# Kernel tuning notes

Hardware: AMD Instinct MI355X
Metric: run time of the kernel (lower is better)

The kernel has to match this reference:

```python
import jax, jax.numpy as jnp
import numpy as np

N_TAPS = 5
N_DELAY = 1
N_ITER = 2
REF_MIC = 0
EPS = 1e-3        # eps passed to ISS updates / divisions
MODEL_EPS = 1e-5  # LaplaceModel internal eps
PB_EPS = 1e-6     # projection_back eps


def _mag_sq(x):
    return jnp.real(x) ** 2 + jnp.imag(x) ** 2


def _div(num, den, eps=EPS):
    # torchiva divide: num / clamp(den, min=eps); den is real
    return num / jnp.maximum(den, eps)


def _laplace_model(Y):
    # Laplace source model: per-source/per-frame weight 1/(2*||y(:,n)||), broadcast over freq
    denom = 2.0 * jnp.sqrt(jnp.sum(_mag_sq(Y), axis=-2, keepdims=True))
    return jnp.broadcast_to(1.0 / jnp.maximum(denom, MODEL_EPS), Y.shape)


def _demix_derev(X, X_bar, W, H):
    reverb = jnp.einsum('...cfdt,...dftn->...cfn', H, X_bar)
    sep = jnp.einsum('...cfd,...dfn->...cfn', W, X)
    return sep - reverb


def _background_update(W, H, C_XX, C_XbarX):
    n_src = W.shape[-3]
    A = (jnp.einsum('...sfc,...cfd->...fsd', W, C_XX)
         + jnp.einsum('...sfdt,...dtfc->...fsc', H, C_XbarX))
    J_H = jnp.linalg.solve(A[..., :n_src], A[..., n_src:])  # (..., f, s, c-s)
    return jnp.moveaxis(jnp.conj(J_H), -1, -3)              # (..., c-s, f, s)


def _demix_background(X, J):
    n_src = J.shape[-1]
    return jnp.einsum('...cfd,...dfn->...cfn', J, X[..., :n_src, :, :]) - X[..., n_src:, :, :]


def _iss_v1(src, X, weights, eps=EPS):
    n_frames = X.shape[-1]
    Xs = X[..., src, :, :]
    v_num = jnp.einsum('...cfn,...cfn,...fn->...cf', weights, X, jnp.conj(Xs)) / n_frames
    v_den = jnp.einsum('...cfn,...fn->...cf', weights, _mag_sq(Xs)) / n_frames
    v = _div(v_num, v_den, eps)
    v_s = 1.0 - 1.0 / jnp.sqrt(jnp.maximum(v_den[..., src, :], eps))
    return v.at[..., src, :].set(v_s.astype(v.dtype))


def _iss_v23(X, Zs, weights, eps=EPS):
    v_num = jnp.einsum('...cfn,...cfn,...fn->...cf', weights, X, jnp.conj(Zs))
    v_den = jnp.einsum('...cfn,...fn->...cf', weights, _mag_sq(Zs))
    return _div(v_num, v_den, eps)


def _iss_updates_with_H(X, X_bar, W, H, weights, J=None, Z=None, eps=EPS):
    n_src = X.shape[-3]
    n_chan = n_src if J is None else n_src + Z.shape[-3]
    n_taps = X_bar.shape[-2]
    # sequential rank-1 source updates (loop-carried; small fixed trip count)
    for src in range(n_src):
        v = _iss_v1(src, X, weights, eps)
        X = X - jnp.einsum('...cf,...fn->...cfn', v, X[..., src, :, :])
        W = W - jnp.einsum('...cf,...fd->...cfd', v, W[..., src, :, :])
        H = H - jnp.einsum('...cf,...fdt->...cfdt', v, H[..., src, :, :, :])
    if Z is not None and J is not None:
        for bak in range(n_chan - n_src):
            v = _iss_v23(X, Z[..., bak, :, :], weights, eps)
            X = X - jnp.einsum('...cf,...fn->...cfn', v, Z[..., bak, :, :])
            W = W.at[..., :n_src].add(-jnp.einsum('...cf,...fd->...cfd', v, J[..., bak, :, :]))
            W = W.at[..., n_src + bak].add(v)
    for src in range(n_chan):
        for tap in range(n_taps):
            Xst = X_bar[..., src, :, tap, :]
            v = _iss_v23(X, Xst, weights, eps)
            X = X - jnp.einsum('...cf,...fn->...cfn', v, Xst)
            H = H.at[..., src, tap].add(v)
    return X, W, H


def _one_iter(Y, X, X_bar, C_XX, C_XbarX, W, H, J, eps=EPS):
    weights = _laplace_model(Y)
    g = jnp.maximum(jnp.mean(_mag_sq(Y), axis=(-2, -1), keepdims=True), eps)
    g_sqrt = jnp.sqrt(g)
    Y = _div(Y, g_sqrt, eps)
    W = _div(W, g_sqrt, eps)
    H = _div(H, g_sqrt[..., None], eps)
    weights = weights * g
    J = _background_update(W, H, C_XX, C_XbarX)
    Z = _demix_background(X, J)
    Y, W, H = _iss_updates_with_H(Y, X_bar, W, H, weights, J=J, Z=Z, eps=eps)
    return Y, W, H, J


def _projection_back(Y, W, J, ref_mic=REF_MIC, eps=PB_EPS):
    # overdetermined branch (n_src < n_chan), ref_mic < n_src
    n_src = Y.shape[-3]
    eye = jnp.eye(n_src, dtype=W.dtype)
    W1, W2 = W[..., :n_src], W[..., n_src:]
    B = jnp.einsum('...sfc,...cfk->...sfk', W2, J) + W1  # (..., s, f, s)
    rhs = eye[:, ref_mic:ref_mic + 1]                    # (s, 1)
    BT = jnp.einsum('...sfc->...fcs', B)                 # (..., f, s, s)
    rhs_b = jnp.broadcast_to(rhs, BT.shape[:-2] + rhs.shape)
    a = jnp.linalg.solve(BT + eps * eye, rhs_b)          # (..., f, s, 1)
    a = jnp.swapaxes(a, -3, -2)                          # (..., s, f, 1)
    return Y * a


def _forward(X, n_src):
    n_chan, n_freq, n_frames = X.shape[-3:]
    batch = X.shape[:-3]
    # delayed copies: X_bar[..., c, f, t, n] = X_pad[..., c, f, n + t]
    X_pad = jnp.pad(X, [(0, 0)] * (X.ndim - 1) + [(N_TAPS + N_DELAY, 0)])
    X_bar = jnp.stack([X_pad[..., t:t + n_frames] for t in range(N_TAPS)], axis=-2)
    C_XX = jnp.einsum('...cfn,...dfn->...cfd', X, jnp.conj(X)) / n_frames
    C_XbarX = jnp.einsum('...dftn,...cfn->...dtfc', X_bar, jnp.conj(X)) / n_frames
    eye = jnp.eye(n_chan, dtype=X.dtype)[:n_src]
    W = jnp.broadcast_to(eye[:, None, :], batch + (n_src, n_freq, n_chan))
    H = jnp.zeros(batch + (n_src, n_freq, n_chan, N_TAPS), dtype=X.dtype)
    J = jnp.zeros(batch + (n_chan - n_src, n_freq, n_src), dtype=X.dtype)
    Y = X[..., :n_src, :, :]
    for _ in range(N_ITER):
        Y, W, H, J = _one_iter(Y, X, X_bar, C_XX, C_XbarX, W, H, J)
    J = _background_update(W, H, C_XX, C_XbarX)
    Y = _demix_derev(X, X_bar, W, H)
    Y = _projection_back(Y, W, J)
    return Y


def setup_inputs():
    key = jax.random.key(0)
    k1, k2 = jax.random.split(key)
    B, n_chan, n_freq, n_frames = 2, 6, 257, 1000
    X_real = jax.random.normal(k1, (B, n_chan, n_freq, n_frames), dtype=jnp.float32)
    X_imag = jax.random.normal(k2, (B, n_chan, n_freq, n_frames), dtype=jnp.float32)
    return {"X_real": X_real, "X_imag": X_imag, "n_src": 2}


def reference(X_real, X_imag, n_src):
    X = jax.lax.complex(X_real, X_imag)
    Y = _forward(X, n_src)  # (B, n_src, n_freq, n_frames) complex
    # real view of the complex output: last axis = (real, imag)
    return jnp.stack([jnp.real(Y), jnp.imag(Y)], axis=-1)
```

## Files before the change

kernel.cpp:

```cpp
#include <hip/hip_runtime.h>
#include <math.h>

#define F_   257
#define N_   1000
#define C_   6
#define S_   2
#define K_   4
#define T_   5
#define DLY  6
#define EPSF 1e-3f
#define MODEL_EPSF 1e-5f
#define PB_EPSD 1e-6
#define NTHR 512

__device__ __forceinline__ float2 cmul(float2 a, float2 b){
  return make_float2(a.x*b.x - a.y*b.y, a.x*b.y + a.y*b.x);
}
__device__ __forceinline__ float2 cadd(float2 a, float2 b){ return make_float2(a.x+b.x, a.y+b.y); }
__device__ __forceinline__ float2 csub(float2 a, float2 b){ return make_float2(a.x-b.x, a.y-b.y); }

struct dc { double x, y; };
__device__ __forceinline__ dc dmul(dc a, dc b){ return dc{a.x*b.x - a.y*b.y, a.x*b.y + a.y*b.x}; }
__device__ __forceinline__ dc dadd(dc a, dc b){ return dc{a.x+b.x, a.y+b.y}; }
__device__ __forceinline__ dc dsub(dc a, dc b){ return dc{a.x-b.x, a.y-b.y}; }
__device__ __forceinline__ dc ddiv(dc a, dc b){
  double d = b.x*b.x + b.y*b.y;
  return dc{(a.x*b.x + a.y*b.y)/d, (a.y*b.x - a.x*b.y)/d};
}
__device__ __forceinline__ dc d_of(float2 a){ return dc{(double)a.x, (double)a.y}; }

struct V2 { float2 v0, v1; };

__global__ __launch_bounds__(128) void k_weights_x(const float* __restrict__ Xre,
    const float* __restrict__ Xim, float* __restrict__ deng, float* __restrict__ gsumg)
{
  __shared__ float redw[2];
  int blk = blockIdx.x;
  int fc = blk & 15; int ch = (blk >> 4) & 7; int s = (blk >> 7) & 1; int b = blk >> 8;
  int tid = threadIdx.x;
  int n = ch*125 + tid;
  int f0 = fc*17, f1 = (f0 + 17 < F_) ? f0 + 17 : F_;
  float acc = 0.f;
  if (tid < 125){
    for (int f = f0; f < f1; ++f){
      size_t gi = ((size_t)(b*C_+s)*F_ + f)*N_ + n;
      float xr = Xre[gi], xi = Xim[gi];
      acc += xr*xr + xi*xi;
    }
    atomicAdd(&deng[(b*S_+s)*N_ + n], acc);
  }
  float r = (tid < 125) ? acc : 0.f;
  #pragma unroll
  for (int off = 32; off; off >>= 1) r += __shfl_xor(r, off);
  if ((tid & 63) == 0) redw[tid >> 6] = r;
  __syncthreads();
  if (tid == 0) atomicAdd(&gsumg[b*S_+s], redw[0] + redw[1]);
}

__global__ __launch_bounds__(128) void k_weights_y(const float2* __restrict__ Yg,
    float* __restrict__ deng, float* __restrict__ gsumg)
{
  __shared__ float redw[2];
  int blk = blockIdx.x;
  int fc = blk & 15; int ch = (blk >> 4) & 7; int s = (blk >> 7) & 1; int b = blk >> 8;
  int tid = threadIdx.x;
  int n = ch*125 + tid;
  int f0 = fc*17, f1 = (f0 + 17 < F_) ? f0 + 17 : F_;
  float acc = 0.f;
  if (tid < 125){
    for (int f = f0; f < f1; ++f){
      float2 y = Yg[(((size_t)(b*F_+f))*S_ + s)*N_ + n];
      acc += y.x*y.x + y.y*y.y;
    }
    atomicAdd(&deng[(b*S_+s)*N_ + n], acc);
  }
  float r = (tid < 125) ? acc : 0.f;
  #pragma unroll
  for (int off = 32; off; off >>= 1) r += __shfl_xor(r, off);
  if ((tid & 63) == 0) redw[tid >> 6] = r;
  __syncthreads();
  if (tid == 0) atomicAdd(&gsumg[b*S_+s], redw[0] + redw[1]);
}

__device__ __forceinline__ void bg_update(int tid, const float2* Wl,
    const float2* Hl, float2* Al, float2* Jl,
    const float2* cx, const float2* cb)
{
  if (tid < S_*C_){
    int s = tid / C_, j = tid - s*C_;
    float2 a = make_float2(0.f, 0.f);
    #pragma unroll
    for (int i = 0; i < C_; ++i) a = cadd(a, cmul(Wl[s*C_+i], cx[i*C_+j]));
    #pragma unroll
    for (int i = 0; i < C_; ++i)
      #pragma unroll
      for (int t = 0; t < T_; ++t)
        a = cadd(a, cmul(Hl[(s*C_+i)*T_+t], cb[(i*T_+t)*C_+j]));
    Al[s*C_+j] = a;
  }
  __syncthreads();
  if (tid == 0){
    dc M00 = d_of(Al[0]),  M01 = d_of(Al[1]);
    dc M10 = d_of(Al[C_]), M11 = d_of(Al[C_+1]);
    dc det = dsub(dmul(M00, M11), dmul(M01, M10));
    #pragma unroll
    for (int k = 0; k < K_; ++k){
      dc r0 = d_of(Al[2+k]), r1 = d_of(Al[C_+2+k]);
      dc x0 = ddiv(dsub(dmul(M11, r0), dmul(M01, r1)), det);
      dc x1 = ddiv(dsub(dmul(M00, r1), dmul(M10, r0)), det);
      Jl[k*S_+0] = make_float2((float)x0.x, (float)(-x0.y));
      Jl[k*S_+1] = make_float2((float)x1.x, (float)(-x1.y));
    }
  }
  __syncthreads();
}

template<typename FS>
__device__ __forceinline__ V2 round2(int tid, bool hasB, int rb, float* redl,
    float2& yA0, float2& yA1, float2& yB0, float2& yB1,
    float wA0, float wA1, float wB0, float wB1,
    FS sf, bool isV1, int src)
{
  float2 sA = sf(0), sB = sf(1);
  float m = sA.x*sA.x + sA.y*sA.y;
  float r0 = wA0*(yA0.x*sA.x + yA0.y*sA.y);
  float r1 = wA0*(yA0.y*sA.x - yA0.x*sA.y);
  float r2 = wA0*m;
  float r3 = wA1*(yA1.x*sA.x + yA1.y*sA.y);
  float r4 = wA1*(yA1.y*sA.x - yA1.x*sA.y);
  float r5 = wA1*m;
  if (hasB){
    float mb = sB.x*sB.x + sB.y*sB.y;
    r0 += wB0*(yB0.x*sB.x + yB0.y*sB.y);
    r1 += wB0*(yB0.y*sB.x - yB0.x*sB.y);
    r2 += wB0*mb;
    r3 += wB1*(yB1.x*sB.x + yB1.y*sB.y);
    r4 += wB1*(yB1.y*sB.x - yB1.x*sB.y);
    r5 += wB1*mb;
  }
  #pragma unroll
  for (int off = 32; off; off >>= 1){
    r0 += __shfl_xor(r0, off); r1 += __shfl_xor(r1, off);
    r2 += __shfl_xor(r2, off); r3 += __shfl_xor(r3, off);
    r4 += __shfl_xor(r4, off); r5 += __shfl_xor(r5, off);
  }
  int lane = tid & 63, wid = tid >> 6;
  if (lane == 0){
    float2* rw = (float2*)(redl + rb*64 + wid*8);
    rw[0] = make_float2(r0, r1);
    rw[1] = make_float2(r2, r3);
    rw[2] = make_float2(r4, r5);
  }
  __syncthreads();
  float pv = ((lane & 7) < 6) ? redl[rb*64 + (lane >> 3)*8 + (lane & 7)] : 0.f;
  pv += __shfl_xor(pv, 8);
  pv += __shfl_xor(pv, 16);
  pv += __shfl_xor(pv, 32);
  float t0 = __shfl(pv, 0), t1 = __shfl(pv, 1), t2 = __shfl(pv, 2);
  float t3 = __shfl(pv, 3), t4 = __shfl(pv, 4), t5 = __shfl(pv, 5);
  if (isV1){
    const float inv = 1.f/(float)N_;
    t0*=inv; t1*=inv; t2*=inv; t3*=inv; t4*=inv; t5*=inv;
  }
  float d0 = fmaxf(t2, EPSF), d1 = fmaxf(t5, EPSF);
  float2 v0 = make_float2(t0/d0, t1/d0);
  float2 v1 = make_float2(t3/d1, t4/d1);
  if (isV1){
    if (src == 0) v0 = make_float2(1.f - 1.f/sqrtf(d0), 0.f);
    else          v1 = make_float2(1.f - 1.f/sqrtf(d1), 0.f);
  }
  yA0 = csub(yA0, cmul(v0, sA)); yA1 = csub(yA1, cmul(v1, sA));
  if (hasB){ yB0 = csub(yB0, cmul(v0, sB)); yB1 = csub(yB1, cmul(v1, sB)); }
  return V2{v0, v1};
}

template<bool FIRST, bool FINAL>
__global__ __launch_bounds__(512, 6) void k_main(const float* __restrict__ Xre,
    const float* __restrict__ Xim, float2* __restrict__ Yg, float2* __restrict__ Wg,
    float2* __restrict__ Hg, float2* __restrict__ Cxxg,
    float2* __restrict__ Cbxg, const float* __restrict__ deng,
    const float* __restrict__ gsumg, float2* __restrict__ out2)
{
  __shared__ float2 Xl[C_*N_];
  __shared__ float2 Wl[S_*C_];
  __shared__ float2 Hl[S_*C_*T_];
  __shared__ float2 Jl[K_*S_];
  __shared__ float2 Al[S_*C_];
  __shared__ float  redl[2*64];
  __shared__ float2 Cxl[C_*C_];
  __shared__ float2 Cbl[C_*T_*C_];

  int p = blockIdx.x; int b = p / F_; int f = p - b*F_;
  int tid = threadIdx.x;
  const int nA = tid;
  const int nB = tid + NTHR;
  const bool hasB = (nB < N_);
  const int nBs = hasB ? nB : 0;

  for (int i = tid; i < C_*N_; i += NTHR){
    int c = i / N_, n = i - c*N_;
    size_t gi = ((size_t)(b*C_+c)*F_ + f)*N_ + n;
    Xl[i] = make_float2(Xre[gi], Xim[gi]);
  }
  if (tid < 128) redl[tid] = 0.f;

  float gv0 = fmaxf(gsumg[b*S_+0] * (1.f/((float)F_*(float)N_)), EPSF);
  float gv1 = fmaxf(gsumg[b*S_+1] * (1.f/((float)F_*(float)N_)), EPSF);
  float ig0 = 1.f / fmaxf(sqrtf(gv0), EPSF);
  float ig1 = 1.f / fmaxf(sqrtf(gv1), EPSF);

  float wA0 = gv0 / fmaxf(2.f*sqrtf(deng[(b*S_+0)*N_+nA]), MODEL_EPSF);
  float wA1 = gv1 / fmaxf(2.f*sqrtf(deng[(b*S_+1)*N_+nA]), MODEL_EPSF);
  float wB0 = 0.f, wB1 = 0.f;
  if (hasB){
    wB0 = gv0 / fmaxf(2.f*sqrtf(deng[(b*S_+0)*N_+nB]), MODEL_EPSF);
    wB1 = gv1 / fmaxf(2.f*sqrtf(deng[(b*S_+1)*N_+nB]), MODEL_EPSF);
  }

  if (FIRST){
    if (tid < S_*C_){
      int s = tid / C_, c = tid - s*C_;
      Wl[tid] = make_float2((s==c) ? (s ? ig1 : ig0) : 0.f, 0.f);
    }
    if (tid < S_*C_*T_) Hl[tid] = make_float2(0.f, 0.f);
  } else {
    if (tid < S_*C_){
      float ig = (tid / C_) ? ig1 : ig0;
      float2 w = Wg[(size_t)p*S_*C_ + tid];
      Wl[tid] = make_float2(w.x*ig, w.y*ig);
    }
    if (tid < S_*C_*T_){
      float ig = (tid / (C_*T_)) ? ig1 : ig0;
      float2 h = Hg[(size_t)p*S_*C_*T_ + tid];
      Hl[tid] = make_float2(h.x*ig, h.y*ig);
    }
  }
  __syncthreads();

  if (FIRST){
    int wid = tid >> 6, lane = tid & 63;
    const float inv_n = 1.0f / (float)N_;
    for (int e = wid; e < 216; e += 8){
      int a_ch, b_ch, lag;
      if (e < 36){ a_ch = e / 6; b_ch = e - a_ch*6; lag = 0; }
      else {
        int i2 = e - 36;
        a_ch = i2 / (T_*C_); int t = (i2 / C_) % T_; b_ch = i2 % C_;
        lag = DLY - t;
      }
      float accx = 0.f, accy = 0.f;
      for (int n = lane; n < N_; n += 64){
        if (n >= lag){
          float2 xa = Xl[a_ch*N_ + n - lag];
          float2 xb = Xl[b_ch*N_ + n];
          accx += xa.x*xb.x + xa.y*xb.y;
          accy += xa.y*xb.x - xa.x*xb.y;
        }
      }
      #pragma unroll
      for (int off = 32; off; off >>= 1){
        accx += __shfl_xor(accx, off);
        accy += __shfl_xor(accy, off);
      }
      if (lane == 0){
        float2 r = make_float2(accx*inv_n, accy*inv_n);
        if (e < 36){ Cxl[e] = r; Cxxg[(size_t)p*(C_*C_) + e] = r; }
        else { Cbl[e-36] = r; Cbxg[(size_t)p*(C_*T_*C_) + (e-36)] = r; }
      }
    }
    __syncthreads();
  }

  const float2* cx = FIRST ? (const float2*)Cxl : (const float2*)(Cxxg + (size_t)p*C_*C_);
  const float2* cb = FIRST ? (const float2*)Cbl : (const float2*)(Cbxg + (size_t)p*C_*T_*C_);

  float2 xA0 = Xl[nA], xA1 = Xl[N_+nA];
  float2 xB0 = make_float2(0.f,0.f), xB1 = make_float2(0.f,0.f);
  if (hasB){ xB0 = Xl[nB]; xB1 = Xl[N_+nB]; }

  float2 yA0, yA1, yB0 = make_float2(0.f,0.f), yB1 = make_float2(0.f,0.f);
  if (FIRST){
    yA0 = make_float2(xA0.x*ig0, xA0.y*ig0);
    yA1 = make_float2(xA1.x*ig1, xA1.y*ig1);
    if (hasB){
      yB0 = make_float2(xB0.x*ig0, xB0.y*ig0);
      yB1 = make_float2(xB1.x*ig1, xB1.y*ig1);
    }
  } else {
    float2 t0 = Yg[((size_t)p*S_+0)*N_+nA];
    float2 t1 = Yg[((size_t)p*S_+1)*N_+nA];
    yA0 = make_float2(t0.x*ig0, t0.y*ig0);
    yA1 = make_float2(t1.x*ig1, t1.y*ig1);
    if (hasB){
      float2 u0 = Yg[((size_t)p*S_+0)*N_+nB];
      float2 u1 = Yg[((size_t)p*S_+1)*N_+nB];
      yB0 = make_float2(u0.x*ig0, u0.y*ig0);
      yB1 = make_float2(u1.x*ig1, u1.y*ig1);
    }
  }

  bg_update(tid, Wl, Hl, Al, Jl, cx, cb);

  int rr = 0;

  for (int src2 = 0; src2 < S_; ++src2){
    V2 v = round2(tid, hasB, (rr++)&1, redl, yA0,yA1,yB0,yB1, wA0,wA1,wB0,wB1,
        [&](int k)->float2 {
          return (src2 == 0) ? (k ? yB0 : yA0) : (k ? yB1 : yA1);
        }, true, src2);
    if (tid < C_){
      float2 ws = Wl[src2*C_+tid];
      Wl[tid]      = csub(Wl[tid],      cmul(v.v0, ws));
      Wl[C_+tid]   = csub(Wl[C_+tid],   cmul(v.v1, ws));
    } else if (tid >= 64 && tid < 64 + C_*T_){
      int i = tid - 64;
      float2 hs = Hl[src2*C_*T_+i];
      Hl[i]        = csub(Hl[i],        cmul(v.v0, hs));
      Hl[C_*T_+i]  = csub(Hl[C_*T_+i],  cmul(v.v1, hs));
    }
  }

  for (int bak = 0; bak < K_; ++bak){
    float2 J0 = Jl[bak*S_+0], J1 = Jl[bak*S_+1];
    V2 v = round2(tid, hasB, (rr++)&1, redl, yA0,yA1,yB0,yB1, wA0,wA1,wB0,wB1,
        [&](int k)->float2 {
          float2 x0 = k ? xB0 : xA0;
          float2 x1 = k ? xB1 : xA1;
          int n = k ? nBs : nA;
          float2 z = cadd(cmul(J0, x0), cmul(J1, x1));
          return csub(z, Xl[(S_+bak)*N_ + n]);
        }, false, 0);
    if (tid < S_){
      float2 vv = tid ? v.v1 : v.v0;
      Wl[tid*C_+0]      = csub(Wl[tid*C_+0], cmul(vv, J0));
      Wl[tid*C_+1]      = csub(Wl[tid*C_+1], cmul(vv, J1));
      Wl[tid*C_+S_+bak] = cadd(Wl[tid*C_+S_+bak], vv);
    }
  }

  for (int sc = 0; sc < C_; ++sc){
    for (int tap = 0; tap < T_; ++tap){
      int lag = DLY - tap;
      V2 v = round2(tid, hasB, (rr++)&1, redl, yA0,yA1,yB0,yB1, wA0,wA1,wB0,wB1,
          [&](int k)->float2 {
            int n = (k ? nBs : nA) - lag;
            return (n >= 0) ? Xl[sc*N_ + n] : make_float2(0.f, 0.f);
          }, false, 0);
      if (tid < S_){
        int idx = (tid*C_+sc)*T_+tap;
        Hl[idx] = cadd(Hl[idx], tid ? v.v1 : v.v0);
      }
    }
  }

  __syncthreads();

  if (!FINAL){
    Yg[((size_t)p*S_+0)*N_+nA] = yA0;
    Yg[((size_t)p*S_+1)*N_+nA] = yA1;
    if (hasB){
      Yg[((size_t)p*S_+0)*N_+nB] = yB0;
      Yg[((size_t)p*S_+1)*N_+nB] = yB1;
    }
    if (tid < S_*C_)    Wg[(size_t)p*S_*C_ + tid]    = Wl[tid];
    if (tid < S_*C_*T_) Hg[(size_t)p*S_*C_*T_ + tid] = Hl[tid];
  } else {
    bg_update(tid, Wl, Hl, Al, Jl, cx, cb);

    float2 oA0 = make_float2(0.f,0.f), oA1 = oA0, oB0 = oA0, oB1 = oA0;
    #pragma unroll
    for (int d = 0; d < C_; ++d){
      float2 x = Xl[d*N_+nA];
      oA0 = cadd(oA0, cmul(Wl[d],    x));
      oA1 = cadd(oA1, cmul(Wl[C_+d], x));
    }
    #pragma unroll
    for (int t = 0; t < T_; ++t){
      int m = nA - (DLY - t);
      if (m >= 0){
        #pragma unroll
        for (int d = 0; d < C_; ++d){
          float2 x = Xl[d*N_+m];
          oA0 = csub(oA0, cmul(Hl[d*T_+t],      x));
          oA1 = csub(oA1, cmul(Hl[(C_+d)*T_+t], x));
        }
      }
    }
    if (hasB){
      #pragma unroll
      for (int d = 0; d < C_; ++d){
        float2 x = Xl[d*N_+nB];
        oB0 = cadd(oB0, cmul(Wl[d],    x));
        oB1 = cadd(oB1, cmul(Wl[C_+d], x));
      }
      #pragma unroll
      for (int t = 0; t < T_; ++t){
        int m = nB - (DLY - t);
        #pragma unroll
        for (int d = 0; d < C_; ++d){
          float2 x = Xl[d*N_+m];
          oB0 = csub(oB0, cmul(Hl[d*T_+t],      x));
          oB1 = csub(oB1, cmul(Hl[(C_+d)*T_+t], x));
        }
      }
    }

    if (tid == 0){
      dc Bm[2][2];
      #pragma unroll
      for (int s2 = 0; s2 < S_; ++s2)
        #pragma unroll
        for (int k = 0; k < S_; ++k){
          dc acc = d_of(Wl[s2*C_+k]);
          #pragma unroll
          for (int c = 0; c < K_; ++c)
            acc = dadd(acc, dmul(d_of(Wl[s2*C_+S_+c]), d_of(Jl[c*S_+k])));
          Bm[s2][k] = acc;
        }
      dc G00 = dc{Bm[0][0].x + PB_EPSD, Bm[0][0].y};
      dc G01 = Bm[1][0];
      dc G10 = Bm[0][1];
      dc G11 = dc{Bm[1][1].x + PB_EPSD, Bm[1][1].y};
      dc det = dsub(dmul(G00, G11), dmul(G01, G10));
      dc a0 = ddiv(G11, det);
      dc a1 = ddiv(dc{-G10.x, -G10.y}, det);
      Al[0] = make_float2((float)a0.x, (float)a0.y);
      Al[1] = make_float2((float)a1.x, (float)a1.y);
    }
    __syncthreads();
    float2 s0 = Al[0], s1 = Al[1];
    out2[((size_t)(b*S_+0)*F_ + f)*N_ + nA] = cmul(oA0, s0);
    out2[((size_t)(b*S_+1)*F_ + f)*N_ + nA] = cmul(oA1, s1);
    if (hasB){
      out2[((size_t)(b*S_+0)*F_ + f)*N_ + nB] = cmul(oB0, s0);
      out2[((size_t)(b*S_+1)*F_ + f)*N_ + nB] = cmul(oB1, s1);
    }
  }
}

extern "C" void kernel_launch(void* const* d_in, const int* in_sizes, int n_in,
                              void* d_out, int out_size, void* d_ws, size_t ws_size,
                              hipStream_t stream)
{
  const float* Xre = (const float*)d_in[0];
  const float* Xim = (const float*)d_in[1];
  int B = in_sizes[0] / (C_*F_*N_);
  int P = B*F_;

  float2* Yg    = (float2*)d_ws;
  float2* Wg    = Yg    + (size_t)P*S_*N_;
  float2* Hg    = Wg    + (size_t)P*S_*C_;
  float2* Cxxg  = Hg    + (size_t)P*S_*C_*T_;
  float2* Cbxg  = Cxxg  + (size_t)P*C_*C_;
  float*  deng0 = (float*)(Cbxg + (size_t)P*C_*T_*C_);
  float*  deng1 = deng0 + (size_t)B*S_*N_;
  float*  gsum0 = deng1 + (size_t)B*S_*N_;
  float*  gsum1 = gsum0 + (size_t)B*S_;
  float2* out2  = (float2*)d_out;

  size_t zeroBytes = (2*(size_t)B*S_*N_ + 2*(size_t)B*S_) * sizeof(float);
  int WG = B*S_*8*16;

  hipMemsetAsync(deng0, 0, zeroBytes, stream);
  k_weights_x<<<WG, 128, 0, stream>>>(Xre, Xim, deng0, gsum0);
  k_main<true,false><<<P, 512, 0, stream>>>(Xre, Xim, Yg, Wg, Hg, Cxxg, Cbxg,
                                            deng0, gsum0, nullptr);
  k_weights_y<<<WG, 128, 0, stream>>>(Yg, deng1, gsum1);
  k_main<false,true><<<P, 512, 0, stream>>>(Xre, Xim, Yg, Wg, Hg, Cxxg, Cbxg,
                                            deng1, gsum1, out2);
}
```

Before: 440.1 us.

## Batch sequential ISS rank-1 updates into Gram-matrix reductions with triangular solve

```diff
diff --git a/kernel.cpp b/kernel.cpp
--- a/kernel.cpp
+++ b/kernel.cpp
@@ -29,7 +29,11 @@
 }
 __device__ __forceinline__ dc d_of(float2 a){ return dc{(double)a.x, (double)a.y}; }
 
-struct V2 { float2 v0, v1; };
+__device__ __forceinline__ float wred(float v){
+  #pragma unroll
+  for (int off = 32; off; off >>= 1) v += __shfl_xor(v, off);
+  return v;
+}
 
 __global__ __launch_bounds__(128) void k_weights_x(const float* __restrict__ Xre,
     const float* __restrict__ Xim, float* __restrict__ deng, float* __restrict__ gsumg)
@@ -115,67 +119,107 @@
   __syncthreads();
 }
 
-template<typename FS>
-__device__ __forceinline__ V2 round2(int tid, bool hasB, int rb, float* redl,
+__device__ __forceinline__ float2 rdc2(const float* c, int i){
+  return make_float2(c[i], c[i+1]);
+}
+
+__device__ __forceinline__ void chainZf(int s, const float* c0, const float* c1, float2* vz)
+{
+  float2 a0=rdc2(c0,0*6+s*3), a1=rdc2(c0,1*6+s*3), a2=rdc2(c0,2*6+s*3), a3=rdc2(c0,3*6+s*3);
+  float D0=c0[0*6+s*3+2], D1=c0[1*6+s*3+2], D2=c0[2*6+s*3+2], D3=c0[3*6+s*3+2];
+  float d;
+  d = fmaxf(D0, EPSF); vz[0] = make_float2(a0.x/d, a0.y/d);
+  a1 = csub(a1, cmul(vz[0], rdc2(c1, 0*4+s*2)));
+  a2 = csub(a2, cmul(vz[0], rdc2(c1, 1*4+s*2)));
+  a3 = csub(a3, cmul(vz[0], rdc2(c1, 2*4+s*2)));
+  d = fmaxf(D1, EPSF); vz[1] = make_float2(a1.x/d, a1.y/d);
+  a2 = csub(a2, cmul(vz[1], rdc2(c1, 3*4+s*2)));
+  a3 = csub(a3, cmul(vz[1], rdc2(c1, 4*4+s*2)));
+  d = fmaxf(D2, EPSF); vz[2] = make_float2(a2.x/d, a2.y/d);
+  a3 = csub(a3, cmul(vz[2], rdc2(c1, 5*4+s*2)));
+  d = fmaxf(D3, EPSF); vz[3] = make_float2(a3.x/d, a3.y/d);
+}
+
+__device__ __forceinline__ void chainTf(int s, const float* c0, const float* c1, float2* vt)
+{
+  float2 a0=rdc2(c0,0*6+s*3), a1=rdc2(c0,1*6+s*3), a2=rdc2(c0,2*6+s*3);
+  float2 a3=rdc2(c0,3*6+s*3), a4=rdc2(c0,4*6+s*3);
+  float D0=c0[0*6+s*3+2], D1=c0[1*6+s*3+2], D2=c0[2*6+s*3+2];
+  float D3=c0[3*6+s*3+2], D4=c0[4*6+s*3+2];
+  float d;
+  d = fmaxf(D0, EPSF); vt[0] = make_float2(a0.x/d, a0.y/d);
+  a1 = csub(a1, cmul(vt[0], rdc2(c1, 0*4+s*2)));
+  a2 = csub(a2, cmul(vt[0], rdc2(c1, 1*4+s*2)));
+  a3 = csub(a3, cmul(vt[0], rdc2(c1, 2*4+s*2)));
+  a4 = csub(a4, cmul(vt[0], rdc2(c1, 3*4+s*2)));
+  d = fmaxf(D1, EPSF); vt[1] = make_float2(a1.x/d, a1.y/d);
+  a2 = csub(a2, cmul(vt[1], rdc2(c1, 4*4+s*2)));
+  a3 = csub(a3, cmul(vt[1], rdc2(c1, 5*4+s*2)));
+  a4 = csub(a4, cmul(vt[1], rdc2(c1, 6*4+s*2)));
+  d = fmaxf(D2, EPSF); vt[2] = make_float2(a2.x/d, a2.y/d);
+  a3 = csub(a3, cmul(vt[2], rdc2(c1, 7*4+s*2)));
+  a4 = csub(a4, cmul(vt[2], rdc2(c1, 8*4+s*2)));
+  d = fmaxf(D3, EPSF); vt[3] = make_float2(a3.x/d, a3.y/d);
+  a4 = csub(a4, cmul(vt[3], rdc2(c1, 9*4+s*2)));
+  d = fmaxf(D4, EPSF); vt[4] = make_float2(a4.x/d, a4.y/d);
+}
+
+template<int SRC>
+__device__ __forceinline__ void src_round_reg(int tid, int lane, int wid,
+    float (*part)[73], float (*comb)[40], float2* Wl, float2* Hl,
     float2& yA0, float2& yA1, float2& yB0, float2& yB1,
-    float wA0, float wA1, float wB0, float wB1,
-    FS sf, bool isV1, int src)
-{
-  float2 sA = sf(0), sB = sf(1);
-  float m = sA.x*sA.x + sA.y*sA.y;
-  float r0 = wA0*(yA0.x*sA.x + yA0.y*sA.y);
-  float r1 = wA0*(yA0.y*sA.x - yA0.x*sA.y);
-  float r2 = wA0*m;
-  float r3 = wA1*(yA1.x*sA.x + yA1.y*sA.y);
-  float r4 = wA1*(yA1.y*sA.x - yA1.x*sA.y);
-  float r5 = wA1*m;
-  if (hasB){
-    float mb = sB.x*sB.x + sB.y*sB.y;
-    r0 += wB0*(yB0.x*sB.x + yB0.y*sB.y);
-    r1 += wB0*(yB0.y*sB.x - yB0.x*sB.y);
-    r2 += wB0*mb;
-    r3 += wB1*(yB1.x*sB.x + yB1.y*sB.y);
-    r4 += wB1*(yB1.y*sB.x - yB1.x*sB.y);
-    r5 += wB1*mb;
-  }
-  #pragma unroll
-  for (int off = 32; off; off >>= 1){
-    r0 += __shfl_xor(r0, off); r1 += __shfl_xor(r1, off);
-    r2 += __shfl_xor(r2, off); r3 += __shfl_xor(r3, off);
-    r4 += __shfl_xor(r4, off); r5 += __shfl_xor(r5, off);
-  }
-  int lane = tid & 63, wid = tid >> 6;
+    float wA0, float wA1, float wB0, float wB1)
+{
+  float2 sA = (SRC==0) ? yA0 : yA1;
+  float2 sB = (SRC==0) ? yB0 : yB1;
+  float m  = sA.x*sA.x + sA.y*sA.y;
+  float mb = sB.x*sB.x + sB.y*sB.y;
+  float r0 = wA0*(yA0.x*sA.x + yA0.y*sA.y) + wB0*(yB0.x*sB.x + yB0.y*sB.y);
+  float r1 = wA0*(yA0.y*sA.x - yA0.x*sA.y) + wB0*(yB0.y*sB.x - yB0.x*sB.y);
+  float r2 = wA0*m + wB0*mb;
+  float r3 = wA1*(yA1.x*sA.x + yA1.y*sA.y) + wB1*(yB1.x*sB.x + yB1.y*sB.y);
+  float r4 = wA1*(yA1.y*sA.x - yA1.x*sA.y) + wB1*(yB1.y*sB.x - yB1.x*sB.y);
+  float r5 = wA1*m + wB1*mb;
+  r0 = wred(r0); r1 = wred(r1); r2 = wred(r2);
+  r3 = wred(r3); r4 = wred(r4); r5 = wred(r5);
   if (lane == 0){
-    float2* rw = (float2*)(redl + rb*64 + wid*8);
-    rw[0] = make_float2(r0, r1);
-    rw[1] = make_float2(r2, r3);
-    rw[2] = make_float2(r4, r5);
-  }
-  __syncthreads();
-  float pv = ((lane & 7) < 6) ? redl[rb*64 + (lane >> 3)*8 + (lane & 7)] : 0.f;
-  pv += __shfl_xor(pv, 8);
-  pv += __shfl_xor(pv, 16);
-  pv += __shfl_xor(pv, 32);
-  float t0 = __shfl(pv, 0), t1 = __shfl(pv, 1), t2 = __shfl(pv, 2);
-  float t3 = __shfl(pv, 3), t4 = __shfl(pv, 4), t5 = __shfl(pv, 5);
-  if (isV1){
-    const float inv = 1.f/(float)N_;
-    t0*=inv; t1*=inv; t2*=inv; t3*=inv; t4*=inv; t5*=inv;
-  }
+    part[wid][0]=r0; part[wid][1]=r1; part[wid][2]=r2;
+    part[wid][3]=r3; part[wid][4]=r4; part[wid][5]=r5;
+  }
+  __syncthreads();
+  if (tid < 6){
+    float s = 0.f;
+    #pragma unroll
+    for (int w = 0; w < 8; ++w) s += part[w][tid];
+    comb[0][tid] = s;
+  }
+  __syncthreads();
+  const float inv = 1.f/(float)N_;
+  float t0=comb[0][0]*inv, t1=comb[0][1]*inv, t2=comb[0][2]*inv;
+  float t3=comb[0][3]*inv, t4=comb[0][4]*inv, t5=comb[0][5]*inv;
   float d0 = fmaxf(t2, EPSF), d1 = fmaxf(t5, EPSF);
   float2 v0 = make_float2(t0/d0, t1/d0);
   float2 v1 = make_float2(t3/d1, t4/d1);
-  if (isV1){
-    if (src == 0) v0 = make_float2(1.f - 1.f/sqrtf(d0), 0.f);
-    else          v1 = make_float2(1.f - 1.f/sqrtf(d1), 0.f);
-  }
-  yA0 = csub(yA0, cmul(v0, sA)); yA1 = csub(yA1, cmul(v1, sA));
-  if (hasB){ yB0 = csub(yB0, cmul(v0, sB)); yB1 = csub(yB1, cmul(v1, sB)); }
-  return V2{v0, v1};
+  if (SRC == 0) v0 = make_float2(1.f - 1.f/sqrtf(d0), 0.f);
+  else          v1 = make_float2(1.f - 1.f/sqrtf(d1), 0.f);
+  yA0 = csub(yA0, cmul(v0, sA));
+  yA1 = csub(yA1, cmul(v1, sA));
+  yB0 = csub(yB0, cmul(v0, sB));
+  yB1 = csub(yB1, cmul(v1, sB));
+  if (tid < C_){
+    float2 ws = Wl[SRC*C_+tid];
+    Wl[tid]    = csub(Wl[tid],    cmul(v0, ws));
+    Wl[C_+tid] = csub(Wl[C_+tid], cmul(v1, ws));
+  } else if (tid >= 64 && tid < 64 + C_*T_){
+    int i = tid - 64;
+    float2 hs = Hl[SRC*C_*T_+i];
+    Hl[i]       = csub(Hl[i],       cmul(v0, hs));
+    Hl[C_*T_+i] = csub(Hl[C_*T_+i], cmul(v1, hs));
+  }
 }
 
 template<bool FIRST, bool FINAL>
-__global__ __launch_bounds__(512, 6) void k_main(const float* __restrict__ Xre,
+__global__ __launch_bounds__(512, 4) void k_main(const float* __restrict__ Xre,
     const float* __restrict__ Xim, float2* __restrict__ Yg, float2* __restrict__ Wg,
     float2* __restrict__ Hg, float2* __restrict__ Cxxg,
     float2* __restrict__ Cbxg, const float* __restrict__ deng,
@@ -186,12 +230,14 @@
   __shared__ float2 Hl[S_*C_*T_];
   __shared__ float2 Jl[K_*S_];
   __shared__ float2 Al[S_*C_];
-  __shared__ float  redl[2*64];
   __shared__ float2 Cxl[C_*C_];
   __shared__ float2 Cbl[C_*T_*C_];
+  __shared__ float  part[8][73];
+  __shared__ float  comb[2][40];
 
   int p = blockIdx.x; int b = p / F_; int f = p - b*F_;
   int tid = threadIdx.x;
+  int lane = tid & 63, wid = tid >> 6;
   const int nA = tid;
   const int nB = tid + NTHR;
   const bool hasB = (nB < N_);
@@ -202,13 +248,88 @@
     size_t gi = ((size_t)(b*C_+c)*F_ + f)*N_ + n;
     Xl[i] = make_float2(Xre[gi], Xim[gi]);
   }
-  if (tid < 128) redl[tid] = 0.f;
 
   float gv0 = fmaxf(gsumg[b*S_+0] * (1.f/((float)F_*(float)N_)), EPSF);
   float gv1 = fmaxf(gsumg[b*S_+1] * (1.f/((float)F_*(float)N_)), EPSF);
   float ig0 = 1.f / fmaxf(sqrtf(gv0), EPSF);
   float ig1 = 1.f / fmaxf(sqrtf(gv1), EPSF);
 
+  if (FIRST){
+    if (tid < S_*C_){
+      int s = tid / C_, c = tid - s*C_;
+      Wl[tid] = make_float2((s==c) ? (s ? ig1 : ig0) : 0.f, 0.f);
+    }
+    if (tid < S_*C_*T_) Hl[tid] = make_float2(0.f, 0.f);
+  } else {
+    if (tid < S_*C_){
+      float ig = (tid / C_) ? ig1 : ig0;
+      float2 w = Wg[(size_t)p*S_*C_ + tid];
+      Wl[tid] = make_float2(w.x*ig, w.y*ig);
+    }
+    if (tid < S_*C_*T_){
+      float ig = (tid / (C_*T_)) ? ig1 : ig0;
+      float2 h = Hg[(size_t)p*S_*C_*T_ + tid];
+      Hl[tid] = make_float2(h.x*ig, h.y*ig);
+    }
+  }
+  __syncthreads();
+
+  if (FIRST){
+    const float inv_n = 1.0f / (float)N_;
+    for (int d = 0; d < C_; ++d){
+      float2 lgA[6], lgB[6];
+      #pragma unroll
+      for (int q = 0; q < 6; ++q){
+        const int lag = (q < 5) ? (DLY - q) : 0;
+        lgA[q] = (nA >= lag) ? Xl[d*N_ + nA - lag] : make_float2(0.f,0.f);
+        lgB[q] = hasB ? Xl[d*N_ + nBs - lag] : make_float2(0.f,0.f);
+      }
+      float acc[72];
+      #pragma unroll
+      for (int v = 0; v < 72; ++v) acc[v] = 0.f;
+      #pragma unroll
+      for (int c2 = 0; c2 < 6; ++c2){
+        float2 bA = Xl[c2*N_ + nA];
+        float2 bB = hasB ? Xl[c2*N_ + nBs] : make_float2(0.f,0.f);
+        #pragma unroll
+        for (int q = 0; q < 6; ++q){
+          acc[c2*12 + q*2]     += lgA[q].x*bA.x + lgA[q].y*bA.y
+                                + lgB[q].x*bB.x + lgB[q].y*bB.y;
+          acc[c2*12 + q*2 + 1] += lgA[q].y*bA.x - lgA[q].x*bA.y
+                                + lgB[q].y*bB.x - lgB[q].x*bB.y;
+        }
+      }
+      #pragma unroll
+      for (int v = 0; v < 72; ++v){
+        float r = wred(acc[v]);
+        if (lane == 0) part[wid][v] = r;
+      }
+      __syncthreads();
+      if (tid < 72){
+        float s = 0.f;
+        #pragma unroll
+        for (int w = 0; w < 8; ++w) s += part[w][tid];
+        s *= inv_n;
+        int c2 = tid / 12, r = tid - c2*12, q = r >> 1, im = r & 1;
+        if (q == 5){
+          ((float*)Cxl)[(d*C_+c2)*2 + im] = s;
+          ((float*)(Cxxg + (size_t)p*(C_*C_)))[(d*C_+c2)*2 + im] = s;
+        } else {
+          int idx = (d*T_ + q)*C_ + c2;
+          ((float*)Cbl)[idx*2 + im] = s;
+          ((float*)(Cbxg + (size_t)p*(C_*T_*C_)))[idx*2 + im] = s;
+        }
+      }
+      __syncthreads();
+    }
+  }
+
+  float2 xA[6], xB[6];
+  #pragma unroll
+  for (int c = 0; c < 6; ++c){
+    xA[c] = Xl[c*N_ + nA];
+    xB[c] = hasB ? Xl[c*N_ + nBs] : make_float2(0.f,0.f);
+  }
   float wA0 = gv0 / fmaxf(2.f*sqrtf(deng[(b*S_+0)*N_+nA]), MODEL_EPSF);
   float wA1 = gv1 / fmaxf(2.f*sqrtf(deng[(b*S_+1)*N_+nA]), MODEL_EPSF);
   float wB0 = 0.f, wB1 = 0.f;
@@ -216,75 +337,13 @@
     wB0 = gv0 / fmaxf(2.f*sqrtf(deng[(b*S_+0)*N_+nB]), MODEL_EPSF);
     wB1 = gv1 / fmaxf(2.f*sqrtf(deng[(b*S_+1)*N_+nB]), MODEL_EPSF);
   }
-
-  if (FIRST){
-    if (tid < S_*C_){
-      int s = tid / C_, c = tid - s*C_;
-      Wl[tid] = make_float2((s==c) ? (s ? ig1 : ig0) : 0.f, 0.f);
-    }
-    if (tid < S_*C_*T_) Hl[tid] = make_float2(0.f, 0.f);
-  } else {
-    if (tid < S_*C_){
-      float ig = (tid / C_) ? ig1 : ig0;
-      float2 w = Wg[(size_t)p*S_*C_ + tid];
-      Wl[tid] = make_float2(w.x*ig, w.y*ig);
-    }
-    if (tid < S_*C_*T_){
-      float ig = (tid / (C_*T_)) ? ig1 : ig0;
-      float2 h = Hg[(size_t)p*S_*C_*T_ + tid];
-      Hl[tid] = make_float2(h.x*ig, h.y*ig);
-    }
-  }
-  __syncthreads();
-
-  if (FIRST){
-    int wid = tid >> 6, lane = tid & 63;
-    const float inv_n = 1.0f / (float)N_;
-    for (int e = wid; e < 216; e += 8){
-      int a_ch, b_ch, lag;
-      if (e < 36){ a_ch = e / 6; b_ch = e - a_ch*6; lag = 0; }
-      else {
-        int i2 = e - 36;
-        a_ch = i2 / (T_*C_); int t = (i2 / C_) % T_; b_ch = i2 % C_;
-        lag = DLY - t;
-      }
-      float accx = 0.f, accy = 0.f;
-      for (int n = lane; n < N_; n += 64){
-        if (n >= lag){
-          float2 xa = Xl[a_ch*N_ + n - lag];
-          float2 xb = Xl[b_ch*N_ + n];
-          accx += xa.x*xb.x + xa.y*xb.y;
-          accy += xa.y*xb.x - xa.x*xb.y;
-        }
-      }
-      #pragma unroll
-      for (int off = 32; off; off >>= 1){
-        accx += __shfl_xor(accx, off);
-        accy += __shfl_xor(accy, off);
-      }
-      if (lane == 0){
-        float2 r = make_float2(accx*inv_n, accy*inv_n);
-        if (e < 36){ Cxl[e] = r; Cxxg[(size_t)p*(C_*C_) + e] = r; }
-        else { Cbl[e-36] = r; Cbxg[(size_t)p*(C_*T_*C_) + (e-36)] = r; }
-      }
-    }
-    __syncthreads();
-  }
-
-  const float2* cx = FIRST ? (const float2*)Cxl : (const float2*)(Cxxg + (size_t)p*C_*C_);
-  const float2* cb = FIRST ? (const float2*)Cbl : (const float2*)(Cbxg + (size_t)p*C_*T_*C_);
-
-  float2 xA0 = Xl[nA], xA1 = Xl[N_+nA];
-  float2 xB0 = make_float2(0.f,0.f), xB1 = make_float2(0.f,0.f);
-  if (hasB){ xB0 = Xl[nB]; xB1 = Xl[N_+nB]; }
-
   float2 yA0, yA1, yB0 = make_float2(0.f,0.f), yB1 = make_float2(0.f,0.f);
   if (FIRST){
-    yA0 = make_float2(xA0.x*ig0, xA0.y*ig0);
-    yA1 = make_float2(xA1.x*ig1, xA1.y*ig1);
+    yA0 = make_float2(xA[0].x*ig0, xA[0].y*ig0);
+    yA1 = make_float2(xA[1].x*ig1, xA[1].y*ig1);
     if (hasB){
-      yB0 = make_float2(xB0.x*ig0, xB0.y*ig0);
-      yB1 = make_float2(xB1.x*ig1, xB1.y*ig1);
+      yB0 = make_float2(xB[0].x*ig0, xB[0].y*ig0);
+      yB1 = make_float2(xB[1].x*ig1, xB[1].y*ig1);
     }
   } else {
     float2 t0 = Yg[((size_t)p*S_+0)*N_+nA];
@@ -299,60 +358,197 @@
     }
   }
 
+  const float2* cx = FIRST ? (const float2*)Cxl : (const float2*)(Cxxg + (size_t)p*C_*C_);
+  const float2* cb = FIRST ? (const float2*)Cbl : (const float2*)(Cbxg + (size_t)p*C_*T_*C_);
+
   bg_update(tid, Wl, Hl, Al, Jl, cx, cb);
 
-  int rr = 0;
-
-  for (int src2 = 0; src2 < S_; ++src2){
-    V2 v = round2(tid, hasB, (rr++)&1, redl, yA0,yA1,yB0,yB1, wA0,wA1,wB0,wB1,
-        [&](int k)->float2 {
-          return (src2 == 0) ? (k ? yB0 : yA0) : (k ? yB1 : yA1);
-        }, true, src2);
-    if (tid < C_){
-      float2 ws = Wl[src2*C_+tid];
-      Wl[tid]      = csub(Wl[tid],      cmul(v.v0, ws));
-      Wl[C_+tid]   = csub(Wl[C_+tid],   cmul(v.v1, ws));
-    } else if (tid >= 64 && tid < 64 + C_*T_){
-      int i = tid - 64;
-      float2 hs = Hl[src2*C_*T_+i];
-      Hl[i]        = csub(Hl[i],        cmul(v.v0, hs));
-      Hl[C_*T_+i]  = csub(Hl[C_*T_+i],  cmul(v.v1, hs));
-    }
-  }
-
-  for (int bak = 0; bak < K_; ++bak){
-    float2 J0 = Jl[bak*S_+0], J1 = Jl[bak*S_+1];
-    V2 v = round2(tid, hasB, (rr++)&1, redl, yA0,yA1,yB0,yB1, wA0,wA1,wB0,wB1,
-        [&](int k)->float2 {
-          float2 x0 = k ? xB0 : xA0;
-          float2 x1 = k ? xB1 : xA1;
-          int n = k ? nBs : nA;
-          float2 z = cadd(cmul(J0, x0), cmul(J1, x1));
-          return csub(z, Xl[(S_+bak)*N_ + n]);
-        }, false, 0);
-    if (tid < S_){
-      float2 vv = tid ? v.v1 : v.v0;
-      Wl[tid*C_+0]      = csub(Wl[tid*C_+0], cmul(vv, J0));
-      Wl[tid*C_+1]      = csub(Wl[tid*C_+1], cmul(vv, J1));
-      Wl[tid*C_+S_+bak] = cadd(Wl[tid*C_+S_+bak], vv);
-    }
-  }
-
-  for (int sc = 0; sc < C_; ++sc){
-    for (int tap = 0; tap < T_; ++tap){
-      int lag = DLY - tap;
-      V2 v = round2(tid, hasB, (rr++)&1, redl, yA0,yA1,yB0,yB1, wA0,wA1,wB0,wB1,
-          [&](int k)->float2 {
-            int n = (k ? nBs : nA) - lag;
-            return (n >= 0) ? Xl[sc*N_ + n] : make_float2(0.f, 0.f);
-          }, false, 0);
-      if (tid < S_){
-        int idx = (tid*C_+sc)*T_+tap;
-        Hl[idx] = cadd(Hl[idx], tid ? v.v1 : v.v0);
-      }
-    }
-  }
-
+  src_round_reg<0>(tid, lane, wid, part, comb, Wl, Hl, yA0,yA1,yB0,yB1, wA0,wA1,wB0,wB1);
+  src_round_reg<1>(tid, lane, wid, part, comb, Wl, Hl, yA0,yA1,yB0,yB1, wA0,wA1,wB0,wB1);
+
+  {
+    float2 zA[4], zB[4];
+    #pragma unroll
+    for (int k = 0; k < 4; ++k){
+      zA[k] = csub(cadd(cmul(Jl[2*k], xA[0]), cmul(Jl[2*k+1], xA[1])), xA[2+k]);
+      zB[k] = csub(cadd(cmul(Jl[2*k], xB[0]), cmul(Jl[2*k+1], xB[1])), xB[2+k]);
+    }
+    {
+      float acc[24];
+      #pragma unroll
+      for (int k = 0; k < 4; ++k){
+        float mA = zA[k].x*zA[k].x + zA[k].y*zA[k].y;
+        float mB = zB[k].x*zB[k].x + zB[k].y*zB[k].y;
+        acc[k*6+0] = wA0*(yA0.x*zA[k].x + yA0.y*zA[k].y) + wB0*(yB0.x*zB[k].x + yB0.y*zB[k].y);
+        acc[k*6+1] = wA0*(yA0.y*zA[k].x - yA0.x*zA[k].y) + wB0*(yB0.y*zB[k].x - yB0.x*zB[k].y);
+        acc[k*6+2] = wA0*mA + wB0*mB;
+        acc[k*6+3] = wA1*(yA1.x*zA[k].x + yA1.y*zA[k].y) + wB1*(yB1.x*zB[k].x + yB1.y*zB[k].y);
+        acc[k*6+4] = wA1*(yA1.y*zA[k].x - yA1.x*zA[k].y) + wB1*(yB1.y*zB[k].x - yB1.x*zB[k].y);
+        acc[k*6+5] = wA1*mA + wB1*mB;
+      }
+      #pragma unroll
+      for (int v = 0; v < 24; ++v){
+        float r = wred(acc[v]);
+        if (lane == 0) part[wid][v] = r;
+      }
+      __syncthreads();
+      if (tid < 24){
+        float s = 0.f;
+        #pragma unroll
+        for (int w = 0; w < 8; ++w) s += part[w][tid];
+        comb[0][tid] = s;
+      }
+      __syncthreads();
+    }
+    {
+      float acc[24];
+      constexpr int ZA_[6] = {0,0,0,1,1,2};
+      constexpr int ZB_[6] = {1,2,3,2,3,3};
+      #pragma unroll
+      for (int q = 0; q < 6; ++q){
+        float2 a1 = zA[ZA_[q]], b1 = zA[ZB_[q]];
+        float2 a2 = zB[ZA_[q]], b2 = zB[ZB_[q]];
+        float prA = a1.x*b1.x + a1.y*b1.y, piA = a1.y*b1.x - a1.x*b1.y;
+        float prB = a2.x*b2.x + a2.y*b2.y, piB = a2.y*b2.x - a2.x*b2.y;
+        acc[q*4+0] = wA0*prA + wB0*prB;
+        acc[q*4+1] = wA0*piA + wB0*piB;
+        acc[q*4+2] = wA1*prA + wB1*prB;
+        acc[q*4+3] = wA1*piA + wB1*piB;
+      }
+      #pragma unroll
+      for (int v = 0; v < 24; ++v){
+        float r = wred(acc[v]);
+        if (lane == 0) part[wid][v] = r;
+      }
+      __syncthreads();
+      if (tid < 24){
+        float s = 0.f;
+        #pragma unroll
+        for (int w = 0; w < 8; ++w) s += part[w][tid];
+        comb[1][tid] = s;
+      }
+      __syncthreads();
+    }
+    {
+      float2 vz0[4], vz1[4];
+      chainZf(0, comb[0], comb[1], vz0);
+      chainZf(1, comb[0], comb[1], vz1);
+      #pragma unroll
+      for (int k = 0; k < 4; ++k){
+        yA0 = csub(yA0, cmul(vz0[k], zA[k]));
+        yA1 = csub(yA1, cmul(vz1[k], zA[k]));
+        yB0 = csub(yB0, cmul(vz0[k], zB[k]));
+        yB1 = csub(yB1, cmul(vz1[k], zB[k]));
+      }
+      if (tid == 0){
+        float2 a0 = cadd(cadd(cmul(vz0[0],Jl[0]), cmul(vz0[1],Jl[2])),
+                         cadd(cmul(vz0[2],Jl[4]), cmul(vz0[3],Jl[6])));
+        float2 a1 = cadd(cadd(cmul(vz0[0],Jl[1]), cmul(vz0[1],Jl[3])),
+                         cadd(cmul(vz0[2],Jl[5]), cmul(vz0[3],Jl[7])));
+        Wl[0] = csub(Wl[0], a0);
+        Wl[1] = csub(Wl[1], a1);
+        Wl[S_+0] = cadd(Wl[S_+0], vz0[0]);
+        Wl[S_+1] = cadd(Wl[S_+1], vz0[1]);
+        Wl[S_+2] = cadd(Wl[S_+2], vz0[2]);
+        Wl[S_+3] = cadd(Wl[S_+3], vz0[3]);
+        float2 b0 = cadd(cadd(cmul(vz1[0],Jl[0]), cmul(vz1[1],Jl[2])),
+                         cadd(cmul(vz1[2],Jl[4]), cmul(vz1[3],Jl[6])));
+        float2 b1 = cadd(cadd(cmul(vz1[0],Jl[1]), cmul(vz1[1],Jl[3])),
+                         cadd(cmul(vz1[2],Jl[5]), cmul(vz1[3],Jl[7])));
+        Wl[C_+0] = csub(Wl[C_+0], b0);
+        Wl[C_+1] = csub(Wl[C_+1], b1);
+        Wl[C_+S_+0] = cadd(Wl[C_+S_+0], vz1[0]);
+        Wl[C_+S_+1] = cadd(Wl[C_+S_+1], vz1[1]);
+        Wl[C_+S_+2] = cadd(Wl[C_+S_+2], vz1[2]);
+        Wl[C_+S_+3] = cadd(Wl[C_+S_+3], vz1[3]);
+      }
+    }
+  }
+
+  for (int c = 0; c < C_; ++c){
+    float2 tlA[5], tlB[5];
+    #pragma unroll
+    for (int t = 0; t < 5; ++t){
+      const int lag = DLY - t;
+      tlA[t] = (nA >= lag) ? Xl[c*N_ + nA - lag] : make_float2(0.f,0.f);
+      tlB[t] = hasB ? Xl[c*N_ + nBs - lag] : make_float2(0.f,0.f);
+    }
+    {
+      float acc[30];
+      #pragma unroll
+      for (int t = 0; t < 5; ++t){
+        float mA = tlA[t].x*tlA[t].x + tlA[t].y*tlA[t].y;
+        float mB = tlB[t].x*tlB[t].x + tlB[t].y*tlB[t].y;
+        acc[t*6+0] = wA0*(yA0.x*tlA[t].x + yA0.y*tlA[t].y) + wB0*(yB0.x*tlB[t].x + yB0.y*tlB[t].y);
+        acc[t*6+1] = wA0*(yA0.y*tlA[t].x - yA0.x*tlA[t].y) + wB0*(yB0.y*tlB[t].x - yB0.x*tlB[t].y);
+        acc[t*6+2] = wA0*mA + wB0*mB;
+        acc[t*6+3] = wA1*(yA1.x*tlA[t].x + yA1.y*tlA[t].y) + wB1*(yB1.x*tlB[t].x + yB1.y*tlB[t].y);
+        acc[t*6+4] = wA1*(yA1.y*tlA[t].x - yA1.x*tlA[t].y) + wB1*(yB1.y*tlB[t].x - yB1.x*tlB[t].y);
+        acc[t*6+5] = wA1*mA + wB1*mB;
+      }
+      #pragma unroll
+      for (int v = 0; v < 30; ++v){
+        float r = wred(acc[v]);
+        if (lane == 0) part[wid][v] = r;
+      }
+      __syncthreads();
+      if (tid < 30){
+        float s = 0.f;
+        #pragma unroll
+        for (int w = 0; w < 8; ++w) s += part[w][tid];
+        comb[0][tid] = s;
+      }
+      __syncthreads();
+    }
+    {
+      float acc[40];
+      constexpr int TA_[10] = {0,0,0,0,1,1,1,2,2,3};
+      constexpr int TB_[10] = {1,2,3,4,2,3,4,3,4,4};
+      #pragma unroll
+      for (int q = 0; q < 10; ++q){
+        float2 a1 = tlA[TA_[q]], b1 = tlA[TB_[q]];
+        float2 a2 = tlB[TA_[q]], b2 = tlB[TB_[q]];
+        float prA = a1.x*b1.x + a1.y*b1.y, piA = a1.y*b1.x - a1.x*b1.y;
+        float prB = a2.x*b2.x + a2.y*b2.y, piB = a2.y*b2.x - a2.x*b2.y;
+        acc[q*4+0] = wA0*prA + wB0*prB;
+        acc[q*4+1] = wA0*piA + wB0*piB;
+        acc[q*4+2] = wA1*prA + wB1*prB;
+        acc[q*4+3] = wA1*piA + wB1*piB;
+      }
+      #pragma unroll
+      for (int v = 0; v < 40; ++v){
+        float r = wred(acc[v]);
+        if (lane == 0) part[wid][v] = r;
+      }
+      __syncthreads();
+      if (tid < 40){
+        float s = 0.f;
+        #pragma unroll
+        for (int w = 0; w < 8; ++w) s += part[w][tid];
+        comb[1][tid] = s;
+      }
+      __syncthreads();
+    }
+    {
+      float2 vt0[5], vt1[5];
+      chainTf(0, comb[0], comb[1], vt0);
+      chainTf(1, comb[0], comb[1], vt1);
+      #pragma unroll
+      for (int t = 0; t < 5; ++t){
+        yA0 = csub(yA0, cmul(vt0[t], tlA[t]));
+        yA1 = csub(yA1, cmul(vt1[t], tlA[t]));
+        yB0 = csub(yB0, cmul(vt0[t], tlB[t]));
+        yB1 = csub(yB1, cmul(vt1[t], tlB[t]));
+      }
+      if (tid == 0){
+        #pragma unroll
+        for (int t = 0; t < 5; ++t){
+          Hl[(0*C_+c)*T_+t] = cadd(Hl[(0*C_+c)*T_+t], vt0[t]);
+          Hl[(1*C_+c)*T_+t] = cadd(Hl[(1*C_+c)*T_+t], vt1[t]);
+        }
+      }
+    }
+  }
   __syncthreads();
 
   if (!FINAL){
@@ -413,8 +609,8 @@
         for (int k = 0; k < S_; ++k){
           dc acc = d_of(Wl[s2*C_+k]);
           #pragma unroll
-          for (int c = 0; c < K_; ++c)
-            acc = dadd(acc, dmul(d_of(Wl[s2*C_+S_+c]), d_of(Jl[c*S_+k])));
+          for (int cc = 0; cc < K_; ++cc)
+            acc = dadd(acc, dmul(d_of(Wl[s2*C_+S_+cc]), d_of(Jl[cc*S_+k])));
           Bm[s2][k] = acc;
         }
       dc G00 = dc{Bm[0][0].x + PB_EPSD, Bm[0][0].y};
```

New measurement: 870.1 us. 1.98x slower.
